# Kernel tuning notes

Hardware: AMD Instinct MI355X
Metric: run time of the kernel (lower is better)

The kernel has to match this reference:

```python
import jax, jax.numpy as jnp
import numpy as np
from jax import lax

MIN_R = 0.01
RADIUS = 0.8
NSAMPLE = 32
PRED_NSAMPLE = 16
TEMPERATURE = 1.0
DIV_COEF = 10.0
GRID3 = 64  # grid_size**3, grid_size=4
EPS = 1e-5


def _ball_query(q, xyz, radius, nsample):
    """q (M,3), xyz (N,3), radius scalar or (M,). Returns idx (M,nsample) int32, empty (M,) bool.
    Mirrors stack ball_query CUDA op: first-found neighbors within radius, padded with first index."""
    N = xyz.shape[0]
    d2 = jnp.sum((q[:, None, :] - xyz[None, :, :]) ** 2, axis=-1)  # (M,N)
    r = jnp.broadcast_to(jnp.asarray(radius, d2.dtype), (q.shape[0],))[:, None]
    valid = d2 < r * r
    score = jnp.where(valid, -jnp.arange(N, dtype=jnp.int32), -(N + 1))
    vals, _ = lax.top_k(score, nsample)  # largest score == smallest valid index
    idx = -vals
    pad = idx == (N + 1)
    idx = jnp.where(pad, idx[:, :1], idx)  # pad with first found neighbor
    empty = pad[:, 0]                       # no neighbor at all
    idx = jnp.where(empty[:, None], 0, idx)
    return idx, empty


def _group(q, xyz, feats, idx, empty):
    """QueryAndGroup gather: relative xyz concat point features; zero empty queries.
    Returns (M, nsample, 3+C)."""
    g_xyz = xyz[idx] - q[:, None, :]
    g = jnp.concatenate([g_xyz, feats[idx]], axis=-1)
    return jnp.where(empty[:, None, None], jnp.zeros((), g.dtype), g)


def _mlp(x, params):
    """Shared 1x1 Conv2d + BatchNorm2d(training stats) + ReLU stack. x: (B,M,S,C)."""
    for W, g, b in params:
        x = jnp.einsum('bmsc,cd->bmsd', x, W)
        mu = x.mean(axis=(0, 1, 2))
        var = x.var(axis=(0, 1, 2))
        x = (x - mu) * lax.rsqrt(var + EPS) * g + b
        x = jax.nn.relu(x)
    return x


def setup_inputs() -> dict:
    key = jax.random.key(0)
    ks = jax.random.split(key, 16)
    B, N, C, R, Croi = 2, 8192, 32, 64, 128
    scene = jnp.array([10.0, 10.0, 4.0], jnp.float32)
    xyz = jax.random.uniform(ks[0], (B, N, 3), jnp.float32) * scene
    features = jax.random.normal(ks[1], (B, N, C), jnp.float32)
    rois = jax.random.uniform(ks[2], (B, R, GRID3, 3), jnp.float32) * scene
    roi_features = jax.random.normal(ks[3], (B, R, Croi), jnp.float32)

    def kaiming(k, fi, fo):
        return jax.random.normal(k, (fi, fo), jnp.float32) * np.float32(np.sqrt(2.0 / fi))

    return {
        'xyz': xyz, 'features': features, 'rois': rois, 'roi_features': roi_features,
        'temperature_decay': jnp.ones((1,), jnp.float32),
        # predict mlp: [32+3, 32, 32]
        'pw0': kaiming(ks[4], 35, 32), 'pg0': jnp.ones(32), 'pb0': jnp.zeros(32),
        'pw1': kaiming(ks[5], 32, 32), 'pg1': jnp.ones(32), 'pb1': jnp.zeros(32),
        # feat mlp: [32+3, 64, 64]
        'fw0': kaiming(ks[6], 35, 64), 'fg0': jnp.ones(64), 'fb0': jnp.zeros(64),
        'fw1': kaiming(ks[7], 64, 64), 'fg1': jnp.ones(64), 'fb1': jnp.zeros(64),
        # predict fc: [32*64 + 128, 1]
        'fcw': kaiming(ks[8], 2176, 1), 'fcb': jnp.zeros(1),
    }


def reference(xyz, features, rois, roi_features, temperature_decay,
              pw0, pg0, pb0, pw1, pg1, pb1,
              fw0, fg0, fb0, fw1, fg1, fb1, fcw, fcb):
    B, num_rois = rois.shape[0], rois.shape[1]
    new_xyz = rois.reshape(B, -1, 3)  # (B, M, 3), M = num_rois*grid^3

    # ---- radius-prediction branch: fixed-radius grouping + MLP + max-pool ----
    idx_p, empty_p = jax.vmap(lambda q, x: _ball_query(q, x, RADIUS, PRED_NSAMPLE))(new_xyz, xyz)
    gp = jax.vmap(_group)(new_xyz, xyz, features, idx_p, empty_p)  # (B,M,S,3+C)
    gp = _mlp(gp, [(pw0, pg0, pb0), (pw1, pg1, pb1)])
    pooled = gp.max(axis=2)                       # (B, M, Cp)
    pooled = pooled.reshape(B, num_rois, -1)      # (B, R, grid^3*Cp)
    res = jnp.concatenate([pooled, roi_features], axis=-1) @ fcw + fcb  # (B,R,1)
    r = jnp.maximum(res / DIV_COEF + RADIUS, MIN_R)
    r_pts = jnp.broadcast_to(r, (B, num_rois, GRID3)).reshape(B, -1)    # (B, M)

    # ---- deformable branch: per-query radius grouping + soft weights ----
    idx_d, empty_d = jax.vmap(lambda q, x, rr: _ball_query(q, x, rr, NSAMPLE))(new_xyz, xyz, r_pts)
    gd = jax.vmap(_group)(new_xyz, xyz, features, idx_d, empty_d)       # (B,M,S,3+C)
    dist = jnp.linalg.norm(gd[..., :3], axis=-1)                        # (B,M,S)
    w = jax.nn.sigmoid((r_pts[..., None] - dist) / (TEMPERATURE * temperature_decay[0]))
    w = jnp.where(empty_d[..., None], jnp.zeros((), w.dtype), w)
    gd = _mlp(gd, [(fw0, fg0, fb0), (fw1, fg1, fb1)])                   # (B,M,S,Cout)
    new_feats = (w[..., None] * gd).max(axis=2)                          # (B,M,Cout)

    return new_xyz.reshape(-1, 3), new_feats.reshape(-1, new_feats.shape[-1])
```

## Files before the change

kernel.cpp:

```cpp
#include <hip/hip_runtime.h>
#include <hip/hip_fp16.h>

#define NB 2
#define NPTS 8192
#define NQ 4096
#define MTOT 8192
#define SP 16
#define SD 32
#define CIN 32
#define CP 32
#define CF 64
#define NROI 128
#define RADIUS_C 0.8f
#define MIN_R_C 0.01f
#define DIV_COEF_C 10.0f

#define INV_CS 1.25f
#define NCX 13
#define NCY 13
#define NCZ 5
#define NCELL (NCX * NCY * NCZ)

__device__ int    g_idx_p[MTOT * SP];
__device__ int    g_empty_p[MTOT];
__device__ int    g_idx_d[MTOT * SD];
__device__ int    g_empty_d[MTOT];
__device__ int    g_cellcnt[NB][NCELL];
__device__ int    g_cellcur[NB][NCELL];
__device__ int    g_cellstart[NB][NCELL + 1];
__device__ float4 g_cellxyzw[NB][NPTS];
__device__ unsigned char g_xa[(size_t)MTOT * SD * CF * 2];
__device__ unsigned char g_xb[(size_t)MTOT * SD * CF * 2];
__device__ float g_psT[CF * 2048];
__device__ float g_pqT[CF * 2048];
__device__ float g_bnscale[4][CF];
__device__ float g_bnshift[4][CF];
__device__ float g_pdot[MTOT];
__device__ float g_rroi[NROI];

__global__ void copy_xyz_kernel(const float* __restrict__ rois, float* __restrict__ out) {
    int i = blockIdx.x * 256 + threadIdx.x;
    if (i < MTOT * 3) out[i] = rois[i];
}

__global__ void grid_zero_kernel() {
    int i = blockIdx.x * 1024 + threadIdx.x;
    if (i < NB * NCELL) ((int*)g_cellcnt)[i] = 0;
}

__device__ __forceinline__ int cell_of(float x, float y, float z) {
    int cx = min(NCX - 1, max(0, (int)floorf(x * INV_CS)));
    int cy = min(NCY - 1, max(0, (int)floorf(y * INV_CS)));
    int cz = min(NCZ - 1, max(0, (int)floorf(z * INV_CS)));
    return (cz * NCY + cy) * NCX + cx;
}

__global__ void grid_count_kernel(const float* __restrict__ xyz) {
    int i = blockIdx.x * 256 + threadIdx.x;
    int b = i >> 13;
    int cell = cell_of(xyz[(size_t)i * 3 + 0], xyz[(size_t)i * 3 + 1], xyz[(size_t)i * 3 + 2]);
    atomicAdd(&g_cellcnt[b][cell], 1);
}

__global__ void grid_prefix_kernel() {
    __shared__ int sc[1024];
    int b = blockIdx.x, tid = threadIdx.x;
    int v = (tid < NCELL) ? g_cellcnt[b][tid] : 0;
    sc[tid] = v;
    __syncthreads();
    for (int off = 1; off < 1024; off <<= 1) {
        int add = (tid >= off) ? sc[tid - off] : 0;
        __syncthreads();
        sc[tid] += add;
        __syncthreads();
    }
    if (tid < NCELL) {
        int excl = sc[tid] - v;
        g_cellstart[b][tid] = excl;
        g_cellcur[b][tid] = excl;
    }
    if (tid == 0) g_cellstart[b][NCELL] = NPTS;
}

__global__ void grid_scatter_kernel(const float* __restrict__ xyz) {
    int i = blockIdx.x * 256 + threadIdx.x;
    int b = i >> 13, il = i & (NPTS - 1);
    float x = xyz[(size_t)i * 3 + 0];
    float y = xyz[(size_t)i * 3 + 1];
    float z = xyz[(size_t)i * 3 + 2];
    int cell = cell_of(x, y, z);
    int pos = atomicAdd(&g_cellcur[b][cell], 1);
    g_cellxyzw[b][pos] = make_float4(x, y, z, __int_as_float(il));
}

template <int NS>
__launch_bounds__(256, 8)
__global__ void bq_grid_kernel(const float* __restrict__ xyz, const float* __restrict__ newxyz) {
    __shared__ int s_epos[4][512];
    int tid = threadIdx.x, wv = tid >> 6, lane = tid & 63;
    int q = blockIdx.x * 4 + wv;
    int b = q >> 12;
    float qx = newxyz[q * 3 + 0], qy = newxyz[q * 3 + 1], qz = newxyz[q * 3 + 2];
    float r = (NS == SP) ? RADIUS_C : g_rroi[q >> 6];
    float r2 = r * r;
    int* idx_out   = (NS == SP) ? g_idx_p   : g_idx_d;
    int* empty_out = (NS == SP) ? g_empty_p : g_empty_d;

    float rp = r + 1e-4f;
    int xlo = max(0, min(NCX - 1, (int)floorf((qx - rp) * INV_CS)));
    int xhi = max(0, min(NCX - 1, (int)floorf((qx + rp) * INV_CS)));
    int ylo = max(0, min(NCY - 1, (int)floorf((qy - rp) * INV_CS)));
    int yhi = max(0, min(NCY - 1, (int)floorf((qy + rp) * INV_CS)));
    int zlo = max(0, min(NCZ - 1, (int)floorf((qz - rp) * INV_CS)));
    int zhi = max(0, min(NCZ - 1, (int)floorf((qz + rp) * INV_CS)));
    int nx = xhi - xlo + 1, ny = yhi - ylo + 1, nz = zhi - zlo + 1;
    int ncell = nx * ny * nz;

    int cstart = 0, ccnt = 0;
    if (lane < ncell) {
        int cx = xlo + (lane % nx);
        int t1 = lane / nx;
        int cy = ylo + (t1 % ny);
        int cz = zlo + (t1 / ny);
        int cell = (cz * NCY + cy) * NCX + cx;
        cstart = g_cellstart[b][cell];
        ccnt = g_cellstart[b][cell + 1] - cstart;
    }
    int incl = ccnt;
#pragma unroll
    for (int off = 1; off < 64; off <<= 1) {
        int n = __shfl_up(incl, off, 64);
        if (lane >= off) incl += n;
    }
    int T = __shfl(incl, 63, 64);
    int pre = incl - ccnt;

    if (ncell > 64 || T > 512) {
        const float* xb = xyz + (size_t)b * NPTS * 3;
        int cnt2 = 0, first_idx = 0;
        for (int g = 0; g < NPTS / 64 && cnt2 < NS; ++g) {
            int p = (g << 6) + lane;
            float dx = qx - xb[3 * p + 0];
            float dy = qy - xb[3 * p + 1];
            float dz = qz - xb[3 * p + 2];
            bool valid = (dx * dx + dy * dy + dz * dz) < r2;
            unsigned long long mask = __ballot(valid);
            if (cnt2 == 0 && mask) first_idx = (g << 6) + (int)__builtin_ctzll(mask);
            int pos = cnt2 + __popcll(mask & ((1ull << lane) - 1ull));
            if (valid && pos < NS) idx_out[q * NS + pos] = p;
            cnt2 += (int)__popcll(mask);
        }
        if (cnt2 == 0) {
            if (lane < NS) idx_out[q * NS + lane] = 0;
            if (lane == 0) empty_out[q] = 1;
        } else {
            int filled = cnt2 < NS ? cnt2 : NS;
            if (lane >= filled && lane < NS) idx_out[q * NS + lane] = first_idx;
            if (lane == 0) empty_out[q] = 0;
        }
        return;
    }

    for (int k = 0; k < ccnt; ++k) s_epos[wv][pre + k] = cstart + k;
    __asm__ volatile("s_waitcnt lgkmcnt(0)" ::: "memory");

    int p[8];
#pragma unroll
    for (int k = 0; k < 8; ++k) {
        int t = k * 64 + lane;
        int pk = 0x7FFFFFFF;
        if (t < T) {
            int e = s_epos[wv][t];
            float4 v = g_cellxyzw[b][e];
            float dx = qx - v.x, dy = qy - v.y, dz = qz - v.z;
            if (dx * dx + dy * dy + dz * dz < r2) pk = __float_as_int(v.w);
        }
        p[k] = pk;
    }

    int lcnt = 0, lmin = 0x7FFFFFFF;
#pragma unroll
    for (int k = 0; k < 8; ++k) {
        if (p[k] != 0x7FFFFFFF) { ++lcnt; lmin = min(lmin, p[k]); }
    }
    int cnt = lcnt, fidx = lmin;
#pragma unroll
    for (int off = 1; off < 64; off <<= 1) {
        cnt += __shfl_xor(cnt, off, 64);
        fidx = min(fidx, __shfl_xor(fidx, off, 64));
    }
    if (cnt == 0) {
        if (lane < NS) idx_out[q * NS + lane] = 0;
        if (lane == 0) empty_out[q] = 1;
        return;
    }
    int thr = 0x7FFFFFFF;
    if (cnt > NS) {
        int lo = 0, hi = NPTS;
        while (lo < hi) {
            int mid = (lo + hi) >> 1;
            int c = 0;
#pragma unroll
            for (int k = 0; k < 8; ++k) c += (p[k] < mid) ? 1 : 0;
#pragma unroll
            for (int off = 1; off < 64; off <<= 1) c += __shfl_xor(c, off, 64);
            if (c >= NS) hi = mid; else lo = mid + 1;
        }
        thr = lo;
    }
    int qc = 0;
#pragma unroll
    for (int k = 0; k < 8; ++k) qc += (p[k] < thr) ? 1 : 0;
    int qincl = qc;
#pragma unroll
    for (int off = 1; off < 64; off <<= 1) {
        int n = __shfl_up(qincl, off, 64);
        if (lane >= off) qincl += n;
    }
    int pos = qincl - qc;
#pragma unroll
    for (int k = 0; k < 8; ++k) {
        if (p[k] < thr) {
            if (pos < NS) idx_out[q * NS + pos] = p[k];
            ++pos;
        }
    }
    if (lane >= cnt && lane < NS) idx_out[q * NS + lane] = fidx;
    if (lane == 0) empty_out[q] = 0;
}

template <int NS, int CH, bool HALF>
__launch_bounds__(128, 4)
__global__ void mlp_passA_kernel(const float* __restrict__ xyz, const float* __restrict__ feats,
                                 const float* __restrict__ newxyz, const float* __restrict__ W0,
                                 void* __restrict__ xout_) {
    constexpr int GSTR = 37;
    constexpr int SST  = CH + 2;
    __shared__ float buf[128 * GSTR];
    __shared__ float ls[128], lq[128];
    int tid = threadIdx.x;
    int rowbase = blockIdx.x * 128;
    int row = rowbase + tid;
    int q = row / NS, b = q >> 12;
    const int* idx_arr = (NS == SP) ? g_idx_p : g_idx_d;
    const int* emp_arr = (NS == SP) ? g_empty_p : g_empty_d;
    {
        float* dst = &buf[tid * GSTR];
        if (emp_arr[q]) {
#pragma unroll
            for (int c = 0; c < 35; ++c) dst[c] = 0.f;
        } else {
            int idx = idx_arr[row];
            const float* xp = xyz + (size_t)b * NPTS * 3 + idx * 3;
            dst[0] = xp[0] - newxyz[q * 3 + 0];
            dst[1] = xp[1] - newxyz[q * 3 + 1];
            dst[2] = xp[2] - newxyz[q * 3 + 2];
            const float4* fp = (const float4*)(feats + (size_t)b * NPTS * CIN + (size_t)idx * CIN);
#pragma unroll
            for (int j = 0; j < 8; ++j) {
                float4 v = fp[j];
                dst[3 + 4 * j + 0] = v.x; dst[3 + 4 * j + 1] = v.y;
                dst[3 + 4 * j + 2] = v.z; dst[3 + 4 * j + 3] = v.w;
            }
        }
    }
    float acc[CH];
#pragma unroll
    for (int ch = 0; ch < CH; ++ch) acc[ch] = 0.f;
    {
        const float* inrow = &buf[tid * GSTR];
        for (int c = 0; c < 35; ++c) {
            float h = inrow[c];
#pragma unroll
            for (int ch = 0; ch < CH; ++ch) acc[ch] = fmaf(h, W0[c * CH + ch], acc[ch]);
        }
    }
    float* xf = (float*)xout_;
    __half* xh = (__half*)xout_;
    float sum = 0.f, sq = 0.f;
#pragma unroll
    for (int p = 0; p < 2; ++p) {
        __syncthreads();
        if ((tid >> 6) == p) {
            float* srow = &buf[(tid & 63) * SST];
#pragma unroll
            for (int ch = 0; ch < CH; ++ch) srow[ch] = acc[ch];
        }
        __syncthreads();
        if (CH == 64) {
            int ch = tid & 63, rg = tid >> 6;
            for (int r = 0; r < 32; ++r) {
                float v = buf[(rg * 32 + r) * SST + ch];
                size_t o = (size_t)(rowbase + p * 64 + rg * 32 + r) * CH + ch;
                if (HALF) xh[o] = __float2half_rn(v); else xf[o] = v;
                sum += v; sq += v * v;
            }
        } else {
            int ch = tid & 31, rg = tid >> 5;
            for (int r = 0; r < 16; ++r) {
                float v = buf[(rg * 16 + r) * SST + ch];
                size_t o = (size_t)(rowbase + p * 64 + rg * 16 + r) * CH + ch;
                if (HALF) xh[o] = __float2half_rn(v); else xf[o] = v;
                sum += v; sq += v * v;
            }
        }
    }
    ls[tid] = sum; lq[tid] = sq;
    __syncthreads();
    if (CH == 64) {
        if (tid < 64) {
            g_psT[tid * 2048 + blockIdx.x] = ls[tid] + ls[64 + tid];
            g_pqT[tid * 2048 + blockIdx.x] = lq[tid] + lq[64 + tid];
        }
    } else {
        if (tid < 32) {
            g_psT[tid * 2048 + blockIdx.x] = ls[tid] + ls[32 + tid] + ls[64 + tid] + ls[96 + tid];
            g_pqT[tid * 2048 + blockIdx.x] = lq[tid] + lq[32 + tid] + lq[64 + tid] + lq[96 + tid];
        }
    }
}

template <int NS, int CH>
__launch_bounds__(128, 4)
__global__ void mlp_passB_kernel(const float* __restrict__ W1, const float* __restrict__ xin,
                                 float* __restrict__ xout, int bn0) {
    constexpr int HSTR = 33;
    constexpr int SST  = CH + 2;
    __shared__ float buf[128 * 37];
    __shared__ float ls[128], lq[128];
    int tid = threadIdx.x;
    int rowbase = blockIdx.x * 128;
    const float* sc0 = g_bnscale[bn0];
    const float* sh0 = g_bnshift[bn0];
    float acc2[CH];
#pragma unroll
    for (int ch = 0; ch < CH; ++ch) acc2[ch] = 0.f;
    const float4* src = (const float4*)xin;
#pragma unroll
    for (int hc = 0; hc < CH / 32; ++hc) {
        if (hc) __syncthreads();
#pragma unroll
        for (int k = 0; k < 8; ++k) {
            int o4 = tid + k * 128;
            int rloc = o4 >> 3, j = o4 & 7;
            int c = 4 * j, gc = hc * 32 + c;
            float4 v = src[(size_t)(rowbase + rloc) * (CH / 4) + hc * 8 + j];
            float* d = &buf[rloc * HSTR + c];
            d[0] = fmaxf(fmaf(v.x, sc0[gc + 0], sh0[gc + 0]), 0.f);
            d[1] = fmaxf(fmaf(v.y, sc0[gc + 1], sh0[gc + 1]), 0.f);
            d[2] = fmaxf(fmaf(v.z, sc0[gc + 2], sh0[gc + 2]), 0.f);
            d[3] = fmaxf(fmaf(v.w, sc0[gc + 3], sh0[gc + 3]), 0.f);
        }
        __syncthreads();
        const float* hrow = &buf[tid * HSTR];
        for (int c = 0; c < 32; ++c) {
            float h = hrow[c];
#pragma unroll
            for (int ch = 0; ch < CH; ++ch)
                acc2[ch] = fmaf(h, W1[(hc * 32 + c) * CH + ch], acc2[ch]);
        }
    }
    float sum = 0.f, sq = 0.f;
#pragma unroll
    for (int p = 0; p < 2; ++p) {
        __syncthreads();
        if ((tid >> 6) == p) {
            float* srow = &buf[(tid & 63) * SST];
#pragma unroll
            for (int ch = 0; ch < CH; ++ch) srow[ch] = acc2[ch];
        }
        __syncthreads();
        int ch = tid & 31, rg = tid >> 5;
        for (int r = 0; r < 16; ++r) {
            float v = buf[(rg * 16 + r) * SST + ch];
            xout[(size_t)(rowbase + p * 64 + rg * 16 + r) * CH + ch] = v;
            sum += v; sq += v * v;
        }
    }
    ls[tid] = sum; lq[tid] = sq;
    __syncthreads();
    if (tid < 32) {
        g_psT[tid * 2048 + blockIdx.x] = ls[tid] + ls[32 + tid] + ls[64 + tid] + ls[96 + tid];
        g_pqT[tid * 2048 + blockIdx.x] = lq[tid] + lq[32 + tid] + lq[64 + tid] + lq[96 + tid];
    }
}

__launch_bounds__(128, 4)
__global__ void mlp_fB_kernel(const float* __restrict__ W1, const __half* __restrict__ xin,
                              __half* __restrict__ xout) {
    __shared__ float fbuf[64 * 66];
    __shared__ float ls[128], lq[128];
    __half* hbuf = (__half*)fbuf;
    unsigned int* w32 = (unsigned int*)fbuf;
    int tid = threadIdx.x;
    int rowbase = blockIdx.x * 128;
    {
        const float4* src = (const float4*)xin;
#pragma unroll
        for (int k = 0; k < 8; ++k) {
            int o4 = tid + k * 128;
            int rloc = o4 >> 3, j = o4 & 7;
            float4 v = src[(size_t)(rowbase + rloc) * 8 + j];
            const unsigned int* s32 = (const unsigned int*)&v;
#pragma unroll
            for (int m = 0; m < 4; ++m) w32[rloc * 33 + 4 * j + m] = s32[m];
        }
    }
    __syncthreads();
    const float* sc0 = g_bnscale[2];
    const float* sh0 = g_bnshift[2];
    float acc2[CF];
#pragma unroll
    for (int ch = 0; ch < CF; ++ch) acc2[ch] = 0.f;
    {
        const __half* hrow = &hbuf[tid * 66];
        for (int c = 0; c < 64; ++c) {
            float h = fmaxf(fmaf(__half2float(hrow[c]), sc0[c], sh0[c]), 0.f);
#pragma unroll
            for (int ch = 0; ch < CF; ++ch)
                acc2[ch] = fmaf(h, W1[c * CF + ch], acc2[ch]);
        }
    }
    float sum = 0.f, sq = 0.f;
#pragma unroll
    for (int p = 0; p < 2; ++p) {
        __syncthreads();
        if ((tid >> 6) == p) {
            float* srow = &fbuf[(tid & 63) * 66];
#pragma unroll
            for (int ch = 0; ch < CF; ++ch) srow[ch] = acc2[ch];
        }
        __syncthreads();
        int ch = tid & 63, rg = tid >> 6;
        for (int r = 0; r < 32; ++r) {
            float v = fbuf[(rg * 32 + r) * 66 + ch];
            xout[(size_t)(rowbase + p * 64 + rg * 32 + r) * CF + ch] = __float2half_rn(v);
            sum += v; sq += v * v;
        }
    }
    ls[tid] = sum; lq[tid] = sq;
    __syncthreads();
    if (tid < 64) {
        g_psT[tid * 2048 + blockIdx.x] = ls[tid] + ls[64 + tid];
        g_pqT[tid * 2048 + blockIdx.x] = lq[tid] + lq[64 + tid];
    }
}

__global__ void passC_f_kernel(const float* __restrict__ xyz, const float* __restrict__ newxyz,
                               const float* __restrict__ td, const __half* __restrict__ xin,
                               float* __restrict__ out) {
    __shared__ float lw[64];
    int tid = threadIdx.x;
    int qpair = blockIdx.x * 2;
    if (tid < 64) {
        int ql = tid >> 5, s = tid & 31;
        int q = qpair + ql;
        float wv = 0.f;
        if (!g_empty_d[q]) {
            int idx = g_idx_d[q * SD + s];
            int b = q >> 12;
            float dx = xyz[(size_t)b * NPTS * 3 + idx * 3 + 0] - newxyz[q * 3 + 0];
            float dy = xyz[(size_t)b * NPTS * 3 + idx * 3 + 1] - newxyz[q * 3 + 1];
            float dz = xyz[(size_t)b * NPTS * 3 + idx * 3 + 2] - newxyz[q * 3 + 2];
            float dist = sqrtf(dx * dx + dy * dy + dz * dz);
            float rq = g_rroi[q >> 6];
            wv = 1.f / (1.f + expf(-(rq - dist) / td[0]));
        }
        lw[tid] = wv;
    }
    __syncthreads();
    int ql = tid >> 6, ch = tid & 63;
    int q = qpair + ql;
    float sc = g_bnscale[3][ch], sh = g_bnshift[3][ch];
    float m = 0.f;
    for (int s = 0; s < SD; ++s) {
        float v = __half2float(xin[((size_t)q * SD + s) * CF + ch]);
        m = fmaxf(m, lw[ql * 32 + s] * fmaxf(fmaf(v, sc, sh), 0.f));
    }
    out[MTOT * 3 + (size_t)q * CF + ch] = m;
}

__global__ void passC_p_kernel(const float* __restrict__ fcw, const float* __restrict__ xin) {
    int tid = threadIdx.x;
    int q = blockIdx.x * 8 + (tid >> 5);
    int ch = tid & 31;
    float sc = g_bnscale[1][ch], sh = g_bnshift[1][ch];
    float m = 0.f;
    for (int s = 0; s < SP; ++s) {
        float v = xin[(size_t)(q * SP + s) * CP + ch] * sc + sh;
        m = fmaxf(m, fmaxf(v, 0.f));
    }
    float pd = m * fcw[(q & 63) * CP + ch];
    for (int off = 16; off > 0; off >>= 1) pd += __shfl_down(pd, off, 32);
    if (ch == 0) g_pdot[q] = pd;
}

__global__ void finalize_kernel(const float* __restrict__ gamma, const float* __restrict__ beta,
                                float n, int layer, int nblocks) {
    __shared__ double l_s[256], l_q[256];
    int ch = blockIdx.x, tid = threadIdx.x;
    double s = 0, q = 0;
    for (int i = tid; i < nblocks; i += 256) { s += g_psT[ch * 2048 + i]; q += g_pqT[ch * 2048 + i]; }
    l_s[tid] = s; l_q[tid] = q; __syncthreads();
    for (int off = 128; off > 0; off >>= 1) {
        if (tid < off) { l_s[tid] += l_s[tid + off]; l_q[tid] += l_q[tid + off]; }
        __syncthreads();
    }
    if (tid == 0) {
        double mu = l_s[0] / (double)n;
        double var = l_q[0] / (double)n - mu * mu;
        if (var < 0) var = 0;
        double sc = (double)gamma[ch] / sqrt(var + 1e-5);
        g_bnscale[layer][ch] = (float)sc;
        g_bnshift[layer][ch] = (float)((double)beta[ch] - mu * sc);
    }
}

__global__ void roi_r_kernel(const float* __restrict__ roif, const float* __restrict__ fcw,
                             const float* __restrict__ fcb) {
    int tid = threadIdx.x;
    int roi = blockIdx.x * 4 + (tid >> 6);
    int lane = tid & 63;
    float acc = g_pdot[roi * 64 + lane]
              + roif[roi * 128 + lane]      * fcw[2048 + lane]
              + roif[roi * 128 + 64 + lane] * fcw[2048 + 64 + lane];
    for (int off = 32; off > 0; off >>= 1) acc += __shfl_down(acc, off, 64);
    if (lane == 0) {
        float res = acc + fcb[0];
        g_rroi[roi] = fmaxf(res / DIV_COEF_C + RADIUS_C, MIN_R_C);
    }
}

extern "C" void kernel_launch(void* const* d_in, const int* in_sizes, int n_in,
                              void* d_out, int out_size, void* d_ws, size_t ws_size,
                              hipStream_t stream) {
    const float* xyz   = (const float*)d_in[0];
    const float* feats = (const float*)d_in[1];
    const float* rois  = (const float*)d_in[2];
    const float* roif  = (const float*)d_in[3];
    const float* td    = (const float*)d_in[4];
    const float* pw0 = (const float*)d_in[5];
    const float* pg0 = (const float*)d_in[6];
    const float* pb0 = (const float*)d_in[7];
    const float* pw1 = (const float*)d_in[8];
    const float* pg1 = (const float*)d_in[9];
    const float* pb1 = (const float*)d_in[10];
    const float* fw0 = (const float*)d_in[11];
    const float* fg0 = (const float*)d_in[12];
    const float* fb0 = (const float*)d_in[13];
    const float* fw1 = (const float*)d_in[14];
    const float* fg1 = (const float*)d_in[15];
    const float* fb1 = (const float*)d_in[16];
    const float* fcw = (const float*)d_in[17];
    const float* fcb = (const float*)d_in[18];
    float* out = (float*)d_out;

    void* xa; hipGetSymbolAddress(&xa, HIP_SYMBOL(g_xa));
    void* xb; hipGetSymbolAddress(&xb, HIP_SYMBOL(g_xb));

    copy_xyz_kernel<<<96, 256, 0, stream>>>(rois, out);

    grid_zero_kernel<<<2, 1024, 0, stream>>>();
    grid_count_kernel<<<64, 256, 0, stream>>>(xyz);
    grid_prefix_kernel<<<2, 1024, 0, stream>>>();
    grid_scatter_kernel<<<64, 256, 0, stream>>>(xyz);

    bq_grid_kernel<SP><<<MTOT / 4, 256, 0, stream>>>(xyz, rois);
    mlp_passA_kernel<SP, CP, false><<<1024, 128, 0, stream>>>(xyz, feats, rois, pw0, xa);
    finalize_kernel<<<CP, 256, 0, stream>>>(pg0, pb0, (float)(MTOT * SP), 0, 1024);
    mlp_passB_kernel<SP, CP><<<1024, 128, 0, stream>>>(pw1, (const float*)xa, (float*)xb, 0);
    finalize_kernel<<<CP, 256, 0, stream>>>(pg1, pb1, (float)(MTOT * SP), 1, 1024);
    passC_p_kernel<<<MTOT / 8, 256, 0, stream>>>(fcw, (const float*)xb);
    roi_r_kernel<<<NROI / 4, 256, 0, stream>>>(roif, fcw, fcb);

    bq_grid_kernel<SD><<<MTOT / 4, 256, 0, stream>>>(xyz, rois);
    mlp_passA_kernel<SD, CF, true><<<2048, 128, 0, stream>>>(xyz, feats, rois, fw0, xa);
    finalize_kernel<<<CF, 256, 0, stream>>>(fg0, fb0, (float)(MTOT * SD), 2, 2048);
    mlp_fB_kernel<<<2048, 128, 0, stream>>>(fw1, (const __half*)xa, (__half*)xb);
    finalize_kernel<<<CF, 256, 0, stream>>>(fg1, fb1, (float)(MTOT * SD), 3, 2048);
    passC_f_kernel<<<MTOT / 2, 128, 0, stream>>>(xyz, rois, td, (const __half*)xb, out);
}
```

Measured before the change: 268.5 us.

## Use packed fp16 dot2 in second deformable MLP layer and widen ball-query grid path

Measured after the change: 267.9 us. Within noise of the previous version (-0.2%).

```diff
diff --git a/kernel.cpp b/kernel.cpp
--- a/kernel.cpp
+++ b/kernel.cpp
@@ -31,6 +31,7 @@
 __device__ float4 g_cellxyzw[NB][NPTS];
 __device__ unsigned char g_xa[(size_t)MTOT * SD * CF * 2];
 __device__ unsigned char g_xb[(size_t)MTOT * SD * CF * 2];
+__device__ unsigned int g_w1h[CF * CF / 2];
 __device__ float g_psT[CF * 2048];
 __device__ float g_pqT[CF * 2048];
 __device__ float g_bnscale[4][CF];
@@ -38,9 +39,36 @@
 __device__ float g_pdot[MTOT];
 __device__ float g_rroi[NROI];
 
+typedef _Float16 h2v __attribute__((ext_vector_type(2)));
+__device__ __forceinline__ float fdot2f(unsigned int a, unsigned int b, float c) {
+#if defined(__has_builtin)
+#if __has_builtin(__builtin_amdgcn_fdot2)
+    h2v ha, hb;
+    ha = *(h2v*)&a; hb = *(h2v*)&b;
+    return __builtin_amdgcn_fdot2(ha, hb, c, false);
+#else
+    __half2 ha = *(__half2*)&a, hb = *(__half2*)&b;
+    float2 fa = __half22float2(ha), fb = __half22float2(hb);
+    return fmaf(fa.x, fb.x, fmaf(fa.y, fb.y, c));
+#endif
+#else
+    __half2 ha = *(__half2*)&a, hb = *(__half2*)&b;
+    float2 fa = __half22float2(ha), fb = __half22float2(hb);
+    return fmaf(fa.x, fb.x, fmaf(fa.y, fb.y, c));
+#endif
+}
+
 __global__ void copy_xyz_kernel(const float* __restrict__ rois, float* __restrict__ out) {
     int i = blockIdx.x * 256 + threadIdx.x;
     if (i < MTOT * 3) out[i] = rois[i];
+}
+
+__global__ void prep_w1_kernel(const float* __restrict__ fw1) {
+    int i = blockIdx.x * 256 + threadIdx.x;
+    if (i >= CF * CF / 2) return;
+    int ch = i >> 5, c2 = i & 31;
+    __half2 h = __floats2half2_rn(fw1[(2 * c2) * CF + ch], fw1[(2 * c2 + 1) * CF + ch]);
+    g_w1h[i] = *(unsigned int*)&h;
 }
 
 __global__ void grid_zero_kernel() {
@@ -96,7 +124,7 @@
 template <int NS>
 __launch_bounds__(256, 8)
 __global__ void bq_grid_kernel(const float* __restrict__ xyz, const float* __restrict__ newxyz) {
-    __shared__ int s_epos[4][512];
+    __shared__ int s_epos[4][1024];
     int tid = threadIdx.x, wv = tid >> 6, lane = tid & 63;
     int q = blockIdx.x * 4 + wv;
     int b = q >> 12;
@@ -116,26 +144,38 @@
     int nx = xhi - xlo + 1, ny = yhi - ylo + 1, nz = zhi - zlo + 1;
     int ncell = nx * ny * nz;
 
-    int cstart = 0, ccnt = 0;
-    if (lane < ncell) {
-        int cx = xlo + (lane % nx);
-        int t1 = lane / nx;
-        int cy = ylo + (t1 % ny);
-        int cz = zlo + (t1 / ny);
-        int cell = (cz * NCY + cy) * NCX + cx;
-        cstart = g_cellstart[b][cell];
-        ccnt = g_cellstart[b][cell + 1] - cstart;
-    }
-    int incl = ccnt;
-#pragma unroll
-    for (int off = 1; off < 64; off <<= 1) {
-        int n = __shfl_up(incl, off, 64);
-        if (lane >= off) incl += n;
-    }
-    int T = __shfl(incl, 63, 64);
-    int pre = incl - ccnt;
-
-    if (ncell > 64 || T > 512) {
+    int T = 0;
+    bool fb = (ncell > 512);
+    if (!fb) {
+        for (int c0 = 0; c0 < ncell; c0 += 64) {
+            int ci = c0 + lane;
+            int cstart = 0, ccnt = 0;
+            if (ci < ncell) {
+                int cx = xlo + (ci % nx);
+                int t1 = ci / nx;
+                int cy = ylo + (t1 % ny);
+                int cz = zlo + (t1 / ny);
+                int cell = (cz * NCY + cy) * NCX + cx;
+                cstart = g_cellstart[b][cell];
+                ccnt = g_cellstart[b][cell + 1] - cstart;
+            }
+            int incl = ccnt;
+#pragma unroll
+            for (int off = 1; off < 64; off <<= 1) {
+                int n = __shfl_up(incl, off, 64);
+                if (lane >= off) incl += n;
+            }
+            int chunkT = __shfl(incl, 63, 64);
+            int pre = T + incl - ccnt;
+            if (T + chunkT <= 1024) {
+                for (int k = 0; k < ccnt; ++k) s_epos[wv][pre + k] = cstart + k;
+            }
+            T += chunkT;
+        }
+        if (T > 1024) fb = true;
+    }
+
+    if (fb) {
         const float* xb = xyz + (size_t)b * NPTS * 3;
         int cnt2 = 0, first_idx = 0;
         for (int g = 0; g < NPTS / 64 && cnt2 < NS; ++g) {
@@ -160,13 +200,11 @@
         }
         return;
     }
-
-    for (int k = 0; k < ccnt; ++k) s_epos[wv][pre + k] = cstart + k;
     __asm__ volatile("s_waitcnt lgkmcnt(0)" ::: "memory");
 
-    int p[8];
-#pragma unroll
-    for (int k = 0; k < 8; ++k) {
+    int p[16];
+#pragma unroll
+    for (int k = 0; k < 16; ++k) {
         int t = k * 64 + lane;
         int pk = 0x7FFFFFFF;
         if (t < T) {
@@ -180,7 +218,7 @@
 
     int lcnt = 0, lmin = 0x7FFFFFFF;
 #pragma unroll
-    for (int k = 0; k < 8; ++k) {
+    for (int k = 0; k < 16; ++k) {
         if (p[k] != 0x7FFFFFFF) { ++lcnt; lmin = min(lmin, p[k]); }
     }
     int cnt = lcnt, fidx = lmin;
@@ -201,7 +239,7 @@
             int mid = (lo + hi) >> 1;
             int c = 0;
 #pragma unroll
-            for (int k = 0; k < 8; ++k) c += (p[k] < mid) ? 1 : 0;
+            for (int k = 0; k < 16; ++k) c += (p[k] < mid) ? 1 : 0;
 #pragma unroll
             for (int off = 1; off < 64; off <<= 1) c += __shfl_xor(c, off, 64);
             if (c >= NS) hi = mid; else lo = mid + 1;
@@ -210,7 +248,7 @@
     }
     int qc = 0;
 #pragma unroll
-    for (int k = 0; k < 8; ++k) qc += (p[k] < thr) ? 1 : 0;
+    for (int k = 0; k < 16; ++k) qc += (p[k] < thr) ? 1 : 0;
     int qincl = qc;
 #pragma unroll
     for (int off = 1; off < 64; off <<= 1) {
@@ -219,7 +257,7 @@
     }
     int pos = qincl - qc;
 #pragma unroll
-    for (int k = 0; k < 8; ++k) {
+    for (int k = 0; k < 16; ++k) {
         if (p[k] < thr) {
             if (pos < NS) idx_out[q * NS + pos] = p[k];
             ++pos;
@@ -386,14 +424,13 @@
 }
 
 __launch_bounds__(128, 4)
-__global__ void mlp_fB_kernel(const float* __restrict__ W1, const __half* __restrict__ xin,
-                              __half* __restrict__ xout) {
-    __shared__ float fbuf[64 * 66];
+__global__ void mlp_fB_kernel(const __half* __restrict__ xin, __half* __restrict__ xout) {
+    __shared__ unsigned int hp[128 * 37];
     __shared__ float ls[128], lq[128];
-    __half* hbuf = (__half*)fbuf;
-    unsigned int* w32 = (unsigned int*)fbuf;
     int tid = threadIdx.x;
     int rowbase = blockIdx.x * 128;
+    const float* sc0 = g_bnscale[2];
+    const float* sh0 = g_bnshift[2];
     {
         const float4* src = (const float4*)xin;
 #pragma unroll
@@ -401,40 +438,59 @@
             int o4 = tid + k * 128;
             int rloc = o4 >> 3, j = o4 & 7;
             float4 v = src[(size_t)(rowbase + rloc) * 8 + j];
-            const unsigned int* s32 = (const unsigned int*)&v;
-#pragma unroll
-            for (int m = 0; m < 4; ++m) w32[rloc * 33 + 4 * j + m] = s32[m];
+            const __half2* ph = (const __half2*)&v;
+            unsigned int* d = &hp[rloc * 37 + 4 * j];
+#pragma unroll
+            for (int m = 0; m < 4; ++m) {
+                float2 f = __half22float2(ph[m]);
+                int gc = 8 * j + 2 * m;
+                float a = fmaxf(fmaf(f.x, sc0[gc + 0], sh0[gc + 0]), 0.f);
+                float bb = fmaxf(fmaf(f.y, sc0[gc + 1], sh0[gc + 1]), 0.f);
+                __half2 hh = __floats2half2_rn(a, bb);
+                d[m] = *(unsigned int*)&hh;
+            }
         }
     }
     __syncthreads();
-    const float* sc0 = g_bnscale[2];
-    const float* sh0 = g_bnshift[2];
     float acc2[CF];
 #pragma unroll
     for (int ch = 0; ch < CF; ++ch) acc2[ch] = 0.f;
     {
-        const __half* hrow = &hbuf[tid * 66];
-        for (int c = 0; c < 64; ++c) {
-            float h = fmaxf(fmaf(__half2float(hrow[c]), sc0[c], sh0[c]), 0.f);
+        const unsigned int* hrow = &hp[tid * 37];
+#pragma unroll
+        for (int c2 = 0; c2 < 32; ++c2) {
+            unsigned int h2 = hrow[c2];
 #pragma unroll
             for (int ch = 0; ch < CF; ++ch)
-                acc2[ch] = fmaf(h, W1[c * CF + ch], acc2[ch]);
-        }
-    }
+                acc2[ch] = fdot2f(h2, g_w1h[ch * 32 + c2], acc2[ch]);
+        }
+    }
+    {
+        unsigned int orow[32];
+#pragma unroll
+        for (int m = 0; m < 32; ++m) {
+            __half2 hh = __floats2half2_rn(acc2[2 * m], acc2[2 * m + 1]);
+            orow[m] = *(unsigned int*)&hh;
+        }
+        uint4* dst = (uint4*)(xout + (size_t)(rowbase + tid) * CF);
+#pragma unroll
+        for (int m = 0; m < 8; ++m)
+            dst[m] = make_uint4(orow[4 * m], orow[4 * m + 1], orow[4 * m + 2], orow[4 * m + 3]);
+    }
+    float* fview = (float*)hp;
     float sum = 0.f, sq = 0.f;
 #pragma unroll
     for (int p = 0; p < 2; ++p) {
         __syncthreads();
         if ((tid >> 6) == p) {
-            float* srow = &fbuf[(tid & 63) * 66];
+            float* srow = &fview[(tid & 63) * 66];
 #pragma unroll
             for (int ch = 0; ch < CF; ++ch) srow[ch] = acc2[ch];
         }
         __syncthreads();
         int ch = tid & 63, rg = tid >> 6;
         for (int r = 0; r < 32; ++r) {
-            float v = fbuf[(rg * 32 + r) * 66 + ch];
-            xout[(size_t)(rowbase + p * 64 + rg * 32 + r) * CF + ch] = __float2half_rn(v);
+            float v = fview[(rg * 32 + r) * 66 + ch];
             sum += v; sq += v * v;
         }
     }
@@ -559,6 +615,7 @@
     void* xb; hipGetSymbolAddress(&xb, HIP_SYMBOL(g_xb));
 
     copy_xyz_kernel<<<96, 256, 0, stream>>>(rois, out);
+    prep_w1_kernel<<<8, 256, 0, stream>>>(fw1);
 
     grid_zero_kernel<<<2, 1024, 0, stream>>>();
     grid_count_kernel<<<64, 256, 0, stream>>>(xyz);
@@ -576,7 +633,7 @@
     bq_grid_kernel<SD><<<MTOT / 4, 256, 0, stream>>>(xyz, rois);
     mlp_passA_kernel<SD, CF, true><<<2048, 128, 0, stream>>>(xyz, feats, rois, fw0, xa);
     finalize_kernel<<<CF, 256, 0, stream>>>(fg0, fb0, (float)(MTOT * SD), 2, 2048);
-    mlp_fB_kernel<<<2048, 128, 0, stream>>>(fw1, (const __half*)xa, (__half*)xb);
+    mlp_fB_kernel<<<2048, 128, 0, stream>>>((const __half*)xa, (__half*)xb);
     finalize_kernel<<<CF, 256, 0, stream>>>(fg1, fb1, (float)(MTOT * SD), 3, 2048);
     passC_f_kernel<<<MTOT / 2, 128, 0, stream>>>(xyz, rois, td, (const __half*)xb, out);
 }
```
